# Optimization experiments

Measured on AMD Instinct MI355X. Metric: run time of the kernel, lower is better.

The kernel has to match this reference:

```python
import jax, jax.numpy as jnp
import numpy as np

N = 100000
E = 600000
D = 164
H = 2
DK = D // H
EDGE_DIM = 16
TIME_DIM = 8
STEP = 30000  # CFG.msg_chunk_edges


def setup_inputs() -> dict:
    key = jax.random.key(0)
    ks = jax.random.split(key, 14)
    q = jax.random.normal(ks[0], (N, D), dtype=jnp.float32)
    k = jax.random.normal(ks[1], (N, D), dtype=jnp.float32)
    v = jax.random.normal(ks[2], (N, D), dtype=jnp.float32)
    edge_index = jax.random.randint(ks[3], (2, E), 0, N, dtype=jnp.int32)
    edge_attr = jax.random.normal(ks[4], (E, EDGE_DIM), dtype=jnp.float32)
    edge_time = jax.random.uniform(ks[5], (E,), dtype=jnp.float32)
    # time_pe: Linear(1, time_dim)
    Wt = jax.random.normal(ks[6], (TIME_DIM, 1), dtype=jnp.float32) * 0.5
    bt = jax.random.normal(ks[7], (TIME_DIM,), dtype=jnp.float32) * 0.1
    # rel_film MLP: Linear(24, 82) -> ReLU -> Linear(82, 328)
    in_dim = EDGE_DIM + TIME_DIM
    W1 = jax.random.normal(ks[8], (D // 2, in_dim), dtype=jnp.float32) * (1.0 / np.sqrt(in_dim))
    b1 = jax.random.normal(ks[9], (D // 2,), dtype=jnp.float32) * 0.05
    W2 = jax.random.normal(ks[10], (2 * D, D // 2), dtype=jnp.float32) * (1.0 / np.sqrt(D // 2))
    b2 = jax.random.normal(ks[11], (2 * D,), dtype=jnp.float32) * 0.05
    rel_bias = jax.random.normal(ks[12], (H,), dtype=jnp.float32) * 0.02
    return {"q": q, "k": k, "v": v, "edge_index": edge_index,
            "edge_attr": edge_attr, "edge_time": edge_time,
            "Wt": Wt, "bt": bt, "W1": W1, "b1": b1, "W2": W2, "b2": b2,
            "rel_bias": rel_bias}


def reference(q, k, v, edge_index, edge_attr, edge_time, Wt, bt, W1, b1, W2, b2, rel_bias):
    n = q.shape[0]
    C = E // STEP  # number of edge chunks; softmax is per-chunk (dim=0 within chunk)
    src = edge_index[0].reshape(C, STEP)
    dst = edge_index[1].reshape(C, STEP)
    Q = q.reshape(n, H, DK)
    K = k.reshape(n, H, DK)
    V = v.reshape(n, H, DK)
    qh = Q[dst]  # [C, STEP, H, DK]
    kh = K[src]
    vh = V[src]
    # FiLM modulation from edge features + time positional encoding
    t_pe = edge_time.reshape(C, STEP, 1) * Wt[:, 0] + bt  # [C, STEP, TIME_DIM]
    feat = jnp.concatenate([edge_attr.reshape(C, STEP, EDGE_DIM), t_pe], axis=-1)
    hmid = jax.nn.relu(jnp.einsum('cef,of->ceo', feat, W1) + b1)
    gb = jnp.einsum('ceo,go->ceg', hmid, W2) + b2  # [C, STEP, 2*D]
    gamma, beta = jnp.split(gb, 2, axis=-1)
    gamma = jnp.tanh(gamma).reshape(C, STEP, H, DK)
    beta = jnp.tanh(beta).reshape(C, STEP, H, DK)
    vh = vh * (1.0 + gamma) + beta
    # attention score + per-chunk softmax over edges (matches torch dim=0 softmax per chunk)
    score = jnp.sum(qh * kh, axis=-1) / np.sqrt(DK).astype(np.float32) + rel_bias  # [C, STEP, H]
    att = jax.nn.softmax(score, axis=1)
    m = (att[..., None] * vh).reshape(C * STEP, D)
    out = jnp.zeros((n, D), dtype=q.dtype).at[dst.reshape(-1)].add(m)
    return out  # dropout is identity in eval mode
```

## Files before the change

### kernel.cpp

```cpp
#include <hip/hip_runtime.h>

#define NN 100000
#define EE 600000
#define DD 164
#define HH 2
#define DKK 82
#define EDIM 16
#define TDIM 8
#define STEP 30000
#define NC 20
#define FEAT 24
#define HID 82
#define NG 41
#define KP 96
#define MP 336
#define NBLK ((EE + 255) / 256)

typedef __attribute__((ext_vector_type(8))) short short8;
typedef __attribute__((ext_vector_type(4))) float floatx4;

__device__ __forceinline__ float fast_tanh(float x) {
    float e = __expf(2.0f * x);
    return 1.0f - 2.0f * __builtin_amdgcn_rcpf(e + 1.0f);
}

__device__ __forceinline__ short f2bf(float f) {
    union { float f; unsigned u; } x; x.f = f;
    unsigned r = x.u + 0x7fffu + ((x.u >> 16) & 1u);
    return (short)(r >> 16);
}


__global__ void __launch_bounds__(256) prep_w2_kernel(
    const float* __restrict__ W2, const float* __restrict__ b2,
    short* __restrict__ W2p, float* __restrict__ b2p)
{
    int idx = blockIdx.x * 256 + threadIdx.x;
    if (idx < MP * KP) {
        int m = idx / KP, kk = idx - m * KP;
        float val = 0.f;
        if (m < 2 * DD && kk < HID) {
            int dth = m >> 1, p = m & 1;
            val = W2[(size_t)(dth + p * DD) * HID + kk];
        }
        W2p[idx] = f2bf(val);
    }
    if (idx < MP) {
        float bv = 0.f;
        if (idx < 2 * DD) { int dth = idx >> 1, p = idx & 1; bv = b2[dth + p * DD]; }
        b2p[idx] = bv;
    }
}


__global__ void __launch_bounds__(256) zero2_kernel(int* __restrict__ a, int* __restrict__ b, int n) {
    int i = blockIdx.x * 256 + threadIdx.x;
    if (i < n) { a[i] = 0; b[i] = 0; }
}

__global__ void __launch_bounds__(256) count_kernel(const int* __restrict__ ei, int* __restrict__ deg) {
    int e = blockIdx.x * 256 + threadIdx.x;
    if (e < EE) atomicAdd(&deg[ei[EE + e]], 1);
}

__global__ void __launch_bounds__(256) scan_kernel(const int* __restrict__ deg, int* __restrict__ off) {
    const int CH = (NN + 255) / 256;
    int t = threadIdx.x;
    int beg = t * CH, end = min(beg + CH, NN);
    int s = 0;
    for (int i = beg; i < end; ++i) s += deg[i];
    __shared__ int sums[256];
    sums[t] = s;
    __syncthreads();
    for (int d = 1; d < 256; d <<= 1) {
        int val = (t >= d) ? sums[t - d] : 0;
        __syncthreads();
        sums[t] += val;
        __syncthreads();
    }
    int run = (t == 0) ? 0 : sums[t - 1];
    for (int i = beg; i < end; ++i) { off[i] = run; run += deg[i]; }
    if (t == 255) off[NN] = run;
}

__global__ void __launch_bounds__(256) fill_kernel(const int* __restrict__ ei,
                                                   const int* __restrict__ off,
                                                   int* __restrict__ cnt,
                                                   int* __restrict__ elist) {
    int e = blockIdx.x * 256 + threadIdx.x;
    if (e >= EE) return;
    int d = ei[EE + e];
    int p = atomicAdd(&cnt[d], 1);
    elist[off[d] + p] = e;
}


__global__ void __launch_bounds__(256) score_kernel(
    const float* __restrict__ q, const float* __restrict__ k,
    const int* __restrict__ ei, const float* __restrict__ rel_bias,
    float* __restrict__ escore)
{
    int e = blockIdx.x * 256 + threadIdx.x;
    if (e >= EE) return;
    int s = ei[e];
    int d = ei[EE + e];
    const float4* qr = (const float4*)(q + (size_t)d * DD);
    const float4* kr = (const float4*)(k + (size_t)s * DD);
    float s0 = 0.f, s1 = 0.f;
    #pragma unroll 4
    for (int i = 0; i < 20; ++i) {
        float4 a = qr[i], b = kr[i];
        s0 += a.x * b.x; s0 += a.y * b.y; s0 += a.z * b.z; s0 += a.w * b.w;
    }
    {
        float4 a = qr[20], b = kr[20];
        s0 += a.x * b.x + a.y * b.y;
        s1 += a.z * b.z + a.w * b.w;
    }
    #pragma unroll 4
    for (int i = 21; i < 41; ++i) {
        float4 a = qr[i], b = kr[i];
        s1 += a.x * b.x; s1 += a.y * b.y; s1 += a.z * b.z; s1 += a.w * b.w;
    }
    const float inv_sqrt = 0.11043152607484654f;
    escore[2 * e]     = __expf(s0 * inv_sqrt + rel_bias[0]);
    escore[2 * e + 1] = __expf(s1 * inv_sqrt + rel_bias[1]);
}

__global__ void __launch_bounds__(256) chunkinv_kernel(
    const float* __restrict__ escore, float* __restrict__ invsum)
{
    int c = blockIdx.x, h = blockIdx.y;
    const float* base = escore + (size_t)c * STEP * 2 + h;
    float acc = 0.f;
    for (int i = threadIdx.x; i < STEP; i += 256) acc += base[2 * i];
    __shared__ float red[256];
    red[threadIdx.x] = acc;
    __syncthreads();
    for (int s2 = 128; s2 > 0; s2 >>= 1) {
        if (threadIdx.x < s2) red[threadIdx.x] += red[threadIdx.x + s2];
        __syncthreads();
    }
    if (threadIdx.x == 0) invsum[c * 2 + h] = 1.0f / red[0];
}

__global__ void __launch_bounds__(256) zero_kernel(float4* __restrict__ p, int n4) {
    int i = blockIdx.x * 256 + threadIdx.x;
    if (i < n4) p[i] = make_float4(0.f, 0.f, 0.f, 0.f);
}


__global__ void __launch_bounds__(256) main_mfma_kernel(
    const float* __restrict__ v, const int* __restrict__ ei,
    const float* __restrict__ edge_attr, const float* __restrict__ edge_time,
    const float* __restrict__ Wt, const float* __restrict__ bt,
    const float* __restrict__ W1, const float* __restrict__ b1,
    const short* __restrict__ W2p, const float* __restrict__ b2p,
    const float* __restrict__ escore, const float* __restrict__ invsum,
    const int* __restrict__ off, const int* __restrict__ elist,
    float* __restrict__ out)
{
    __shared__ short hmid_lds[256 * KP];
    __shared__ float res_lds[256 * 8];
    __shared__ int   sdst[256];
    __shared__ int   ssrc[256];
    __shared__ float satt[512];

    const int tid = threadIdx.x;
    const int gid = blockIdx.x * 256 + tid;
    const bool valid = gid < EE;
    const int gi = valid ? gid : (EE - 1);
    const int e = elist[gi];
    const int s = ei[e];
    const int d = ei[EE + e];
    sdst[tid] = valid ? d : -1;
    ssrc[tid] = s;
    {
        unsigned c = (unsigned)e / STEP;
        satt[2 * tid]     = escore[2 * e]     * invsum[2 * c];
        satt[2 * tid + 1] = escore[2 * e + 1] * invsum[2 * c + 1];
    }

    float feat[FEAT];
    const float4* ea4 = (const float4*)(edge_attr + (size_t)e * EDIM);
    #pragma unroll
    for (int i = 0; i < 4; ++i) {
        float4 a = ea4[i];
        feat[4 * i + 0] = a.x; feat[4 * i + 1] = a.y;
        feat[4 * i + 2] = a.z; feat[4 * i + 3] = a.w;
    }
    float t = edge_time[e];
    #pragma unroll
    for (int j = 0; j < TDIM; ++j) feat[EDIM + j] = t * Wt[j] + bt[j];

    #pragma unroll 1
    for (int oc = 0; oc < KP / 8; ++oc) {
        union { short h[8]; int4 v4; } pk;
        #pragma unroll
        for (int j = 0; j < 8; ++j) {
            int o = oc * 8 + j;
            float acc = 0.f;
            if (o < HID) {
                acc = b1[o];
                #pragma unroll
                for (int f = 0; f < FEAT; ++f) acc = fmaf(feat[f], W1[o * FEAT + f], acc);
                acc = fmaxf(acc, 0.f);
            }
            pk.h[j] = f2bf(acc);
        }
        *(int4*)&hmid_lds[tid * KP + oc * 8] = pk.v4;
    }
    __syncthreads();

    const int lane = tid & 63;
    const int wavebase = tid & ~63;
    const int lrow = lane & 15;
    const int quad = lane >> 4;

    short8 bfrag[4][3];
    #pragma unroll
    for (int nt = 0; nt < 4; ++nt)
        #pragma unroll
        for (int ks = 0; ks < 3; ++ks)
            bfrag[nt][ks] = *(const short8*)&hmid_lds[(wavebase + nt * 16 + lrow) * KP + ks * 32 + quad * 8];

    bool leader = valid && (tid == 0 || sdst[tid - 1] != d);
    int seglen = 0;
    bool interior = false;
    float* orow = nullptr;
    if (leader) {
        while (tid + seglen < 256 && sdst[tid + seglen] == d) ++seglen;
        int bs = blockIdx.x * 256;
        interior = (off[d] >= bs) && (off[d + 1] <= bs + 256);
        orow = out + (size_t)d * DD;
    }

    #pragma unroll 1
    for (int mt = 0; mt < 21; ++mt) {
        short8 afrag[3];
        #pragma unroll
        for (int ks = 0; ks < 3; ++ks)
            afrag[ks] = *(const short8*)&W2p[(mt * 16 + lrow) * KP + ks * 32 + quad * 8];

        floatx4 acc[4];
        #pragma unroll
        for (int nt = 0; nt < 4; ++nt) acc[nt] = (floatx4)(0.f);
        #pragma unroll
        for (int ks = 0; ks < 3; ++ks)
            #pragma unroll
            for (int nt = 0; nt < 4; ++nt)
                acc[nt] = __builtin_amdgcn_mfma_f32_16x16x32_bf16(afrag[ks], bfrag[nt][ks], acc[nt], 0, 0, 0);

        float4 bias = *(const float4*)&b2p[mt * 16 + quad * 4];
        int d0 = mt * 8 + quad * 2;

        #pragma unroll
        for (int nt = 0; nt < 4; ++nt) {
            int e_loc = wavebase + nt * 16 + lrow;
            float r0 = 0.f, r1 = 0.f;
            if (d0 < DD) {
                float g0  = fast_tanh(acc[nt][0] + bias.x);
                float be0 = fast_tanh(acc[nt][1] + bias.y);
                float g1  = fast_tanh(acc[nt][2] + bias.z);
                float be1 = fast_tanh(acc[nt][3] + bias.w);
                int s_e = ssrc[e_loc];
                const float* vp = v + (size_t)s_e * DD + d0;
                float v0 = vp[0], v1 = vp[1];
                float a0 = satt[2 * e_loc + (d0 >= DKK ? 1 : 0)];
                float a1 = satt[2 * e_loc + (d0 + 1 >= DKK ? 1 : 0)];
                r0 = a0 * (v0 * (1.f + g0) + be0);
                r1 = a1 * (v1 * (1.f + g1) + be1);
            }
            res_lds[e_loc * 8 + quad * 2]     = r0;
            res_lds[e_loc * 8 + quad * 2 + 1] = r1;
        }
        __syncthreads();

        if (leader) {
            float4 s0 = make_float4(0.f, 0.f, 0.f, 0.f);
            float4 s1 = make_float4(0.f, 0.f, 0.f, 0.f);
            for (int t2 = 0; t2 < seglen; ++t2) {
                const float4* rp = (const float4*)&res_lds[(tid + t2) * 8];
                float4 a = rp[0], b = rp[1];
                s0.x += a.x; s0.y += a.y; s0.z += a.z; s0.w += a.w;
                s1.x += b.x; s1.y += b.y; s1.z += b.z; s1.w += b.w;
            }
            int D0 = mt * 8;
            if (interior) {
                *(float4*)(orow + D0) = s0;
                if (D0 + 4 < DD) *(float4*)(orow + D0 + 4) = s1;
            } else {
                unsafeAtomicAdd(orow + D0 + 0, s0.x);
                unsafeAtomicAdd(orow + D0 + 1, s0.y);
                unsafeAtomicAdd(orow + D0 + 2, s0.z);
                unsafeAtomicAdd(orow + D0 + 3, s0.w);
                if (D0 + 4 < DD) {
                    unsafeAtomicAdd(orow + D0 + 4, s1.x);
                    unsafeAtomicAdd(orow + D0 + 5, s1.y);
                    unsafeAtomicAdd(orow + D0 + 6, s1.z);
                    unsafeAtomicAdd(orow + D0 + 7, s1.w);
                }
            }
        }
        __syncthreads();
    }
}


__global__ void __launch_bounds__(256) main_atomic_kernel(
    const float* __restrict__ v, const int* __restrict__ ei,
    const float* __restrict__ edge_attr, const float* __restrict__ edge_time,
    const float* __restrict__ Wt, const float* __restrict__ bt,
    const float* __restrict__ W1, const float* __restrict__ b1,
    const float* __restrict__ W2, const float* __restrict__ b2,
    const float* __restrict__ escore, const float* __restrict__ invsum,
    float* __restrict__ out)
{
    int e = blockIdx.x * 256 + threadIdx.x;
    if (e >= EE) return;
    int s = ei[e];
    int d = ei[EE + e];
    float feat[FEAT];
    const float4* ea4 = (const float4*)(edge_attr + (size_t)e * EDIM);
    #pragma unroll
    for (int i = 0; i < 4; ++i) {
        float4 a = ea4[i];
        feat[4 * i + 0] = a.x; feat[4 * i + 1] = a.y;
        feat[4 * i + 2] = a.z; feat[4 * i + 3] = a.w;
    }
    float t = edge_time[e];
    #pragma unroll
    for (int j = 0; j < TDIM; ++j) feat[EDIM + j] = t * Wt[j] + bt[j];
    float hmid[HID];
    #pragma unroll
    for (int o = 0; o < HID; ++o) {
        float acc = b1[o];
        #pragma unroll
        for (int f = 0; f < FEAT; ++f) acc = fmaf(feat[f], W1[o * FEAT + f], acc);
        hmid[o] = fmaxf(acc, 0.f);
    }
    int c = e / STEP;
    float att0 = escore[2 * e]     * invsum[2 * c];
    float att1 = escore[2 * e + 1] * invsum[2 * c + 1];
    const float4* vrow4 = (const float4*)(v + (size_t)s * DD);
    float* orow = out + (size_t)d * DD;
    #pragma unroll 1
    for (int j = 0; j < NG; ++j) {
        float4 vv = vrow4[j];
        float vvals[4] = {vv.x, vv.y, vv.z, vv.w};
        float res[4];
        #pragma unroll
        for (int u = 0; u < 4; ++u) {
            int dd = 4 * j + u;
            float ga = b2[dd];
            float bb = b2[dd + DD];
            #pragma unroll
            for (int o = 0; o < HID; ++o) {
                ga = fmaf(hmid[o], W2[dd * HID + o], ga);
                bb = fmaf(hmid[o], W2[(dd + DD) * HID + o], bb);
            }
            float gamma = fast_tanh(ga);
            float beta  = fast_tanh(bb);
            float vh = vvals[u] * (1.f + gamma) + beta;
            res[u] = ((dd < DKK) ? att0 : att1) * vh;
        }
        unsafeAtomicAdd(orow + 4 * j + 0, res[0]);
        unsafeAtomicAdd(orow + 4 * j + 1, res[1]);
        unsafeAtomicAdd(orow + 4 * j + 2, res[2]);
        unsafeAtomicAdd(orow + 4 * j + 3, res[3]);
    }
}


extern "C" void kernel_launch(void* const* d_in, const int* in_sizes, int n_in,
                              void* d_out, int out_size, void* d_ws, size_t ws_size,
                              hipStream_t stream) {
    const float* q   = (const float*)d_in[0];
    const float* k   = (const float*)d_in[1];
    const float* v   = (const float*)d_in[2];
    const int*   ei  = (const int*)d_in[3];
    const float* ea  = (const float*)d_in[4];
    const float* et  = (const float*)d_in[5];
    const float* Wt  = (const float*)d_in[6];
    const float* bt  = (const float*)d_in[7];
    const float* W1  = (const float*)d_in[8];
    const float* b1  = (const float*)d_in[9];
    const float* W2  = (const float*)d_in[10];
    const float* b2  = (const float*)d_in[11];
    const float* rb  = (const float*)d_in[12];
    float* out = (float*)d_out;

    short* W2p    = (short*)d_ws;
    float* b2p    = (float*)(W2p + MP * KP);
    float* escore = b2p + MP;
    float* invsum = escore + (size_t)2 * EE;
    int*   deg    = (int*)(invsum + 64);
    int*   off    = deg + NN;
    int*   cnt    = off + NN + 1;
    int*   elist  = cnt + NN;

    size_t need = (size_t)(MP * KP) * 2 + (MP + 2 * EE + 64) * 4 +
                  ((size_t)3 * NN + 1 + EE) * 4;

    int n4 = out_size / 4;
    zero_kernel<<<(n4 + 255) / 256, 256, 0, stream>>>((float4*)out, n4);

    if (ws_size >= need) {
        prep_w2_kernel<<<(MP * KP + 255) / 256, 256, 0, stream>>>(W2, b2, W2p, b2p);
        score_kernel<<<NBLK, 256, 0, stream>>>(q, k, ei, rb, escore);
        chunkinv_kernel<<<dim3(NC, HH), 256, 0, stream>>>(escore, invsum);
        zero2_kernel<<<(NN + 255) / 256, 256, 0, stream>>>(deg, cnt, NN);
        count_kernel<<<NBLK, 256, 0, stream>>>(ei, deg);
        scan_kernel<<<1, 256, 0, stream>>>(deg, off);
        fill_kernel<<<NBLK, 256, 0, stream>>>(ei, off, cnt, elist);
        main_mfma_kernel<<<NBLK, 256, 0, stream>>>(
            v, ei, ea, et, Wt, bt, W1, b1, W2p, b2p, escore, invsum, off, elist, out);
    } else {
        float* escore_f = (float*)d_ws;
        float* invsum_f = escore_f + (size_t)2 * EE;
        score_kernel<<<NBLK, 256, 0, stream>>>(q, k, ei, rb, escore_f);
        chunkinv_kernel<<<dim3(NC, HH), 256, 0, stream>>>(escore_f, invsum_f);
        main_atomic_kernel<<<NBLK, 256, 0, stream>>>(
            v, ei, ea, et, Wt, bt, W1, b1, W2, b2, escore_f, invsum_f, out);
    }
}
```

Baseline: 1.075 ms.

## Double-buffer reduction LDS, hoist gathers, and score edges in dst-sorted order

The main kernel now overlays the hmid buffer with a double-buffered result array, which removes the second barrier per output tile. The source index and attention weights are hoisted into registers, and the v values are prefetched as float2 before the MFMA so the load latency overlaps the matrix math. The score kernel now runs after the CSR build and walks edges in destination-sorted order, so consecutive threads reuse the same q rows in cache. The added cost is an extra elist indirection and scattered escore writes.

```diff
diff --git a/kernel.cpp b/kernel.cpp
--- a/kernel.cpp
+++ b/kernel.cpp
@@ -95,6 +95,39 @@
 }
 
 
+__global__ void __launch_bounds__(256) score_sorted_kernel(
+    const float* __restrict__ q, const float* __restrict__ k,
+    const int* __restrict__ ei, const float* __restrict__ rel_bias,
+    const int* __restrict__ elist, float* __restrict__ escore)
+{
+    int i = blockIdx.x * 256 + threadIdx.x;
+    if (i >= EE) return;
+    int e = elist[i];
+    int s = ei[e];
+    int d = ei[EE + e];
+    const float4* qr = (const float4*)(q + (size_t)d * DD);
+    const float4* kr = (const float4*)(k + (size_t)s * DD);
+    float s0 = 0.f, s1 = 0.f;
+    #pragma unroll 4
+    for (int j = 0; j < 20; ++j) {
+        float4 a = qr[j], b = kr[j];
+        s0 += a.x * b.x; s0 += a.y * b.y; s0 += a.z * b.z; s0 += a.w * b.w;
+    }
+    {
+        float4 a = qr[20], b = kr[20];
+        s0 += a.x * b.x + a.y * b.y;
+        s1 += a.z * b.z + a.w * b.w;
+    }
+    #pragma unroll 4
+    for (int j = 21; j < 41; ++j) {
+        float4 a = qr[j], b = kr[j];
+        s1 += a.x * b.x; s1 += a.y * b.y; s1 += a.z * b.z; s1 += a.w * b.w;
+    }
+    const float inv_sqrt = 0.11043152607484654f;
+    escore[2 * e]     = __expf(s0 * inv_sqrt + rel_bias[0]);
+    escore[2 * e + 1] = __expf(s1 * inv_sqrt + rel_bias[1]);
+}
+
 __global__ void __launch_bounds__(256) score_kernel(
     const float* __restrict__ q, const float* __restrict__ k,
     const int* __restrict__ ei, const float* __restrict__ rel_bias,
@@ -150,6 +183,11 @@
 }
 
 
+union ShOverlay {
+    short hmid[256 * KP];
+    float res[2][256 * 8];
+};
+
 __global__ void __launch_bounds__(256) main_mfma_kernel(
     const float* __restrict__ v, const int* __restrict__ ei,
     const float* __restrict__ edge_attr, const float* __restrict__ edge_time,
@@ -160,8 +198,7 @@
     const int* __restrict__ off, const int* __restrict__ elist,
     float* __restrict__ out)
 {
-    __shared__ short hmid_lds[256 * KP];
-    __shared__ float res_lds[256 * 8];
+    __shared__ ShOverlay sh;
     __shared__ int   sdst[256];
     __shared__ int   ssrc[256];
     __shared__ float satt[512];
@@ -208,7 +245,7 @@
             }
             pk.h[j] = f2bf(acc);
         }
-        *(int4*)&hmid_lds[tid * KP + oc * 8] = pk.v4;
+        *(int4*)&sh.hmid[tid * KP + oc * 8] = pk.v4;
     }
     __syncthreads();
 
@@ -222,7 +259,17 @@
     for (int nt = 0; nt < 4; ++nt)
         #pragma unroll
         for (int ks = 0; ks < 3; ++ks)
-            bfrag[nt][ks] = *(const short8*)&hmid_lds[(wavebase + nt * 16 + lrow) * KP + ks * 32 + quad * 8];
+            bfrag[nt][ks] = *(const short8*)&sh.hmid[(wavebase + nt * 16 + lrow) * KP + ks * 32 + quad * 8];
+
+    int   s_e[4];
+    float a0h[4], a1h[4];
+    #pragma unroll
+    for (int nt = 0; nt < 4; ++nt) {
+        int e_loc = wavebase + nt * 16 + lrow;
+        s_e[nt] = ssrc[e_loc];
+        a0h[nt] = satt[2 * e_loc];
+        a1h[nt] = satt[2 * e_loc + 1];
+    }
 
     bool leader = valid && (tid == 0 || sdst[tid - 1] != d);
     int seglen = 0;
@@ -235,8 +282,21 @@
         orow = out + (size_t)d * DD;
     }
 
+    __syncthreads();
+
+    int p = 0;
     #pragma unroll 1
     for (int mt = 0; mt < 21; ++mt) {
+        const int d0 = mt * 8 + quad * 2;
+        const bool dok = d0 < DD;
+
+        float2 vv[4];
+        #pragma unroll
+        for (int nt = 0; nt < 4; ++nt) {
+            if (dok) vv[nt] = *(const float2*)(v + (size_t)s_e[nt] * DD + d0);
+            else     vv[nt] = make_float2(0.f, 0.f);
+        }
+
         short8 afrag[3];
         #pragma unroll
         for (int ks = 0; ks < 3; ++ks)
@@ -252,27 +312,23 @@
                 acc[nt] = __builtin_amdgcn_mfma_f32_16x16x32_bf16(afrag[ks], bfrag[nt][ks], acc[nt], 0, 0, 0);
 
         float4 bias = *(const float4*)&b2p[mt * 16 + quad * 4];
-        int d0 = mt * 8 + quad * 2;
+        const bool hi = d0 >= DKK;
 
         #pragma unroll
         for (int nt = 0; nt < 4; ++nt) {
             int e_loc = wavebase + nt * 16 + lrow;
             float r0 = 0.f, r1 = 0.f;
-            if (d0 < DD) {
+            if (dok) {
                 float g0  = fast_tanh(acc[nt][0] + bias.x);
                 float be0 = fast_tanh(acc[nt][1] + bias.y);
                 float g1  = fast_tanh(acc[nt][2] + bias.z);
                 float be1 = fast_tanh(acc[nt][3] + bias.w);
-                int s_e = ssrc[e_loc];
-                const float* vp = v + (size_t)s_e * DD + d0;
-                float v0 = vp[0], v1 = vp[1];
-                float a0 = satt[2 * e_loc + (d0 >= DKK ? 1 : 0)];
-                float a1 = satt[2 * e_loc + (d0 + 1 >= DKK ? 1 : 0)];
-                r0 = a0 * (v0 * (1.f + g0) + be0);
-                r1 = a1 * (v1 * (1.f + g1) + be1);
+                float a = hi ? a1h[nt] : a0h[nt];
+                r0 = a * (vv[nt].x * (1.f + g0) + be0);
+                r1 = a * (vv[nt].y * (1.f + g1) + be1);
             }
-            res_lds[e_loc * 8 + quad * 2]     = r0;
-            res_lds[e_loc * 8 + quad * 2 + 1] = r1;
+            sh.res[p][e_loc * 8 + quad * 2]     = r0;
+            sh.res[p][e_loc * 8 + quad * 2 + 1] = r1;
         }
         __syncthreads();
 
@@ -280,7 +336,7 @@
             float4 s0 = make_float4(0.f, 0.f, 0.f, 0.f);
             float4 s1 = make_float4(0.f, 0.f, 0.f, 0.f);
             for (int t2 = 0; t2 < seglen; ++t2) {
-                const float4* rp = (const float4*)&res_lds[(tid + t2) * 8];
+                const float4* rp = (const float4*)&sh.res[p][(tid + t2) * 8];
                 float4 a = rp[0], b = rp[1];
                 s0.x += a.x; s0.y += a.y; s0.z += a.z; s0.w += a.w;
                 s1.x += b.x; s1.y += b.y; s1.z += b.z; s1.w += b.w;
@@ -302,7 +358,7 @@
                 }
             }
         }
-        __syncthreads();
+        p ^= 1;
     }
 }
 
@@ -407,12 +463,12 @@
 
     if (ws_size >= need) {
         prep_w2_kernel<<<(MP * KP + 255) / 256, 256, 0, stream>>>(W2, b2, W2p, b2p);
-        score_kernel<<<NBLK, 256, 0, stream>>>(q, k, ei, rb, escore);
-        chunkinv_kernel<<<dim3(NC, HH), 256, 0, stream>>>(escore, invsum);
         zero2_kernel<<<(NN + 255) / 256, 256, 0, stream>>>(deg, cnt, NN);
         count_kernel<<<NBLK, 256, 0, stream>>>(ei, deg);
         scan_kernel<<<1, 256, 0, stream>>>(deg, off);
         fill_kernel<<<NBLK, 256, 0, stream>>>(ei, off, cnt, elist);
+        score_sorted_kernel<<<NBLK, 256, 0, stream>>>(q, k, ei, rb, elist, escore);
+        chunkinv_kernel<<<dim3(NC, HH), 256, 0, stream>>>(escore, invsum);
         main_mfma_kernel<<<NBLK, 256, 0, stream>>>(
             v, ei, ea, et, Wt, bt, W1, b1, W2p, b2p, escore, invsum, off, elist, out);
     } else {
```

Result: faster. 1.034 ms (-3.8%).
